# Optimization experiments

Hardware: AMD Instinct MI355X
Metric: run time of the kernel (lower is better)

The kernel has to match this reference:

```python
import jax, jax.numpy as jnp
import numpy as np

D_MODEL, D_STATE, D_CONV, EXPAND = 1024, 16, 4, 2
D_INNER = D_MODEL * EXPAND
BATCH, SEQ_LEN = 2, 2048
LN_EPS = 1e-5


def setup_inputs() -> dict:
    key = jax.random.key(0)
    ks = jax.random.split(key, 10)
    s = lambda fan_in: 1.0 / np.sqrt(fan_in)
    x = jax.random.normal(ks[0], (BATCH, D_MODEL, SEQ_LEN), jnp.float32)
    ln_w = jnp.ones((D_MODEL,), jnp.float32)
    ln_b = jnp.zeros((D_MODEL,), jnp.float32)
    # Linear weights stored as [in, out]
    W_in = jax.random.normal(ks[1], (D_MODEL, 2 * D_INNER), jnp.float32) * s(D_MODEL)
    conv_w = jax.random.normal(ks[2], (D_INNER, 1, D_CONV), jnp.float32) * s(D_CONV)
    conv_b = jax.random.normal(ks[3], (D_INNER,), jnp.float32) * s(D_CONV)
    W_x = jax.random.normal(ks[4], (D_INNER, 2 * D_STATE + D_INNER), jnp.float32) * s(D_INNER)
    W_dt = jax.random.normal(ks[5], (D_INNER, D_INNER), jnp.float32) * s(D_INNER)
    b_dt = jax.random.normal(ks[6], (D_INNER,), jnp.float32) * s(D_INNER)
    A_log = jnp.broadcast_to(jnp.log(jnp.arange(1, D_STATE + 1, dtype=jnp.float32))[None, :], (D_INNER, D_STATE))
    Dskip = jnp.ones((D_INNER,), jnp.float32)
    W_out = jax.random.normal(ks[7], (D_INNER, D_MODEL), jnp.float32) * s(D_INNER)
    return {"x": x, "ln_w": ln_w, "ln_b": ln_b, "W_in": W_in, "conv_w": conv_w,
            "conv_b": conv_b, "W_x": W_x, "W_dt": W_dt, "b_dt": b_dt,
            "A_log": A_log, "Dskip": Dskip, "W_out": W_out}


def _selective_scan(u, delta, A, Bp, Cp, Dskip):
    # u, delta: [B, d_inner, L]; A: [d_inner, d_state]; Bp, Cp: [B, d_state, L]
    u_T = jnp.transpose(u, (2, 0, 1))        # [L, B, d_inner]
    d_T = jnp.transpose(delta, (2, 0, 1))    # [L, B, d_inner]
    B_T = jnp.transpose(Bp, (2, 0, 1))       # [L, B, d_state]
    C_T = jnp.transpose(Cp, (2, 0, 1))       # [L, B, d_state]
    h0 = jnp.zeros((u.shape[0], u.shape[1], A.shape[1]), u.dtype)

    def step(h, inp):
        dlt_t, B_t, C_t, u_t = inp
        dA = jnp.exp(dlt_t[..., None] * A)                       # [B, d_inner, d_state]
        h = dA * h + dlt_t[..., None] * B_t[:, None, :] * u_t[..., None]
        y_t = jnp.einsum('bds,bs->bd', h, C_t)
        return h, y_t

    _, ys = jax.lax.scan(step, h0, (d_T, B_T, C_T, u_T))
    y = jnp.transpose(ys, (1, 2, 0))  # [B, d_inner, L]
    return y + Dskip[None, :, None] * u


def reference(x, ln_w, ln_b, W_in, conv_w, conv_b, W_x, W_dt, b_dt, A_log, Dskip, W_out):
    residual = x
    xt = jnp.swapaxes(x, 1, 2)  # [B, L, d_model]
    mu = xt.mean(-1, keepdims=True)
    var = ((xt - mu) ** 2).mean(-1, keepdims=True)
    xn = (xt - mu) * jax.lax.rsqrt(var + LN_EPS) * ln_w + ln_b
    xz = xn @ W_in                                   # [B, L, 2*d_inner]
    xb, z = jnp.split(xz, 2, axis=-1)
    xb = jnp.swapaxes(xb, 1, 2)                      # [B, d_inner, L]
    # causal depthwise conv (torch pads d_conv-1 both sides then slices [:L])
    xb = jax.lax.conv_general_dilated(
        xb, conv_w, window_strides=(1,), padding=[(D_CONV - 1, 0)],
        dimension_numbers=('NCH', 'OIH', 'NCH'), feature_group_count=D_INNER)
    xb = xb + conv_b[None, :, None]
    xb = jax.nn.silu(xb)
    xbt = jnp.swapaxes(xb, 1, 2)                     # [B, L, d_inner]
    bcd = xbt @ W_x                                  # [B, L, 2*d_state + d_inner]
    Bp = bcd[..., :D_STATE]
    Cp = bcd[..., D_STATE:2 * D_STATE]
    dlt = jax.nn.softplus(bcd[..., 2 * D_STATE:] @ W_dt + b_dt)
    Bp = jnp.swapaxes(Bp, 1, 2)                      # [B, d_state, L]
    Cp = jnp.swapaxes(Cp, 1, 2)
    dlt = jnp.swapaxes(dlt, 1, 2)                    # [B, d_inner, L]
    A = -jnp.exp(A_log)
    y = _selective_scan(xb, dlt, A, Bp, Cp, Dskip)   # [B, d_inner, L]
    y = jnp.swapaxes(y, 1, 2) * jax.nn.silu(z)       # [B, L, d_inner]
    out = y @ W_out                                  # [B, L, d_model]
    return jnp.swapaxes(out, 1, 2) + residual
```

## Files before the change

kernel.cpp:

```cpp
#include <hip/hip_runtime.h>
#include <cstdint>
#include <cstddef>

#define SEQL 2048
#define DMODEL 1024
#define DINNER 2048
#define NSTATE 16
#define NC 32
#define TC 64
#define KS 16
#define KCH 128

typedef __attribute__((ext_vector_type(4))) float f32x4;
typedef __attribute__((ext_vector_type(8))) short short8;
typedef __attribute__((ext_vector_type(4))) short short4v;
typedef unsigned short u16;

__device__ __forceinline__ float b2f(u16 u) {
  union { unsigned int i; float f; } v; v.i = ((unsigned int)u) << 16; return v.f;
}
__device__ __forceinline__ u16 f2b(float f) {
  union { float f; unsigned int i; } v; v.f = f;
  unsigned int r = v.i + 0x7FFFu + ((v.i >> 16) & 1u);
  return (u16)(r >> 16);
}

__global__ __launch_bounds__(256) void k_transpose_cvt(
    const float* __restrict__ in, u16* __restrict__ out, int R, int C, int c0) {
  __shared__ float t[32][33];
  int cb = blockIdx.x * 32, rb = blockIdx.y * 32;
  int tx = threadIdx.x, ty = threadIdx.y;
#pragma unroll
  for (int i = 0; i < 32; i += 8)
    t[ty + i][tx] = in[(size_t)(rb + ty + i) * C + c0 + cb + tx];
  __syncthreads();
#pragma unroll
  for (int i = 0; i < 32; i += 8)
    out[(size_t)(cb + ty + i) * R + rb + tx] = f2b(t[tx][ty + i]);
}

__global__ __launch_bounds__(256) void k_cvt_rows(
    const float* __restrict__ in, u16* __restrict__ out) {
  size_t idx = (size_t)blockIdx.x * 256 + threadIdx.x;
  size_t i4 = idx * 4;
  int r = (int)(i4 >> 11), c = (int)(i4 & 2047);
  f32x4 v = *(const f32x4*)&in[(size_t)r * 2080 + 32 + c];
  short4v o;
#pragma unroll
  for (int j = 0; j < 4; ++j) o[j] = (short)f2b(v[j]);
  *(short4v*)&out[i4] = o;
}

__global__ __launch_bounds__(256) void k_layernorm(
    const u16* __restrict__ xt, const float* __restrict__ w,
    const float* __restrict__ b, u16* __restrict__ xn) {
  int row = blockIdx.x;
  const u16* px = xt + (size_t)row * DMODEL;
  int i4 = threadIdx.x * 4;
  short4v sv = *(const short4v*)&px[i4];
  float v[4];
#pragma unroll
  for (int j = 0; j < 4; ++j) v[j] = b2f((u16)sv[j]);
  float s1 = v[0] + v[1] + v[2] + v[3];
  float s2 = v[0]*v[0] + v[1]*v[1] + v[2]*v[2] + v[3]*v[3];
#pragma unroll
  for (int off = 32; off > 0; off >>= 1) {
    s1 += __shfl_xor(s1, off);
    s2 += __shfl_xor(s2, off);
  }
  __shared__ float a1[4], a2[4];
  int lane = threadIdx.x & 63, wid = threadIdx.x >> 6;
  if (lane == 0) { a1[wid] = s1; a2[wid] = s2; }
  __syncthreads();
  float t1 = a1[0] + a1[1] + a1[2] + a1[3];
  float t2 = a2[0] + a2[1] + a2[2] + a2[3];
  float mu = t1 * (1.f / DMODEL);
  float rs = rsqrtf(t2 * (1.f / DMODEL) - mu * mu + 1e-5f);
  short4v ov;
#pragma unroll
  for (int j = 0; j < 4; ++j) ov[j] = (short)f2b((v[j] - mu) * rs * w[i4 + j] + b[i4 + j]);
  *(short4v*)&xn[(size_t)row * DMODEL + i4] = ov;
}

template<int EPI>
__global__ __launch_bounds__(256) void gemm8p(
    const u16* __restrict__ A, const u16* __restrict__ BT,
    void* __restrict__ outp, const float* __restrict__ bias,
    const float* __restrict__ resid, int M, int N, int K) {
  constexpr int LDSTILE = 2 * 128 * 64;
  __shared__ u16 lds[2 * LDSTILE];

  const int tid = threadIdx.x;
  const int w = tid >> 6, lane = tid & 63;
  const int wm = w >> 1, wn = w & 1;
  const int lg = lane >> 4, lr = lane & 15;
  const int wbase = tid & ~63;

  const int gx = N / 128;
  const int cpx = gridDim.x >> 3;
  const int wg = ((int)blockIdx.x & 7) * cpx + ((int)blockIdx.x >> 3);
  const int tm = (wg / gx) * 128;
  const int tn = (wg % gx) * 128;
  const int NT = K >> 6;

  const u16* aSp[2];
  const u16* bSp[2];
  int aD[2], bD[2];
#pragma unroll
  for (int j = 0; j < 2; ++j) {
    int t8 = j * 256 + tid;
    int r8 = t8 >> 3;
    int pr = (r8 & 31) + ((r8 >> 5) << 6);
    int sk = ((((t8 & 7) << 4) ^ ((pr & 7) << 4)) >> 1);
    aSp[j] = A + (size_t)(tm + pr) * K + sk;
    bSp[j] = BT + (size_t)(tn + pr) * K + sk;
    int r8b = (j * 256 + wbase) >> 3;
    int prb = (r8b & 31) + ((r8b >> 5) << 6);
    aD[j] = prb * 64;
    bD[j] = 128 * 64 + prb * 64;
  }
  int aFo[4][2], bFo[4][2];
#pragma unroll
  for (int mf = 0; mf < 4; ++mf)
#pragma unroll
    for (int kk = 0; kk < 2; ++kk) {
      int r = wm * 64 + mf * 16 + lr;
      aFo[mf][kk] = r * 128 + ((kk * 64 + lg * 16) ^ ((r & 7) << 4));
      int rb = wn * 64 + mf * 16 + lr;
      bFo[mf][kk] = 128 * 64 * 2 + rb * 128 + ((kk * 64 + lg * 16) ^ ((rb & 7) << 4));
    }

  auto stA = [&](int toff, int h, int buf) {
#pragma unroll
    for (int j = 0; j < 2; ++j)
      __builtin_amdgcn_global_load_lds(
          (const __attribute__((address_space(1))) void*)(aSp[j] + toff * 64 + h * (K << 5)),
          (__attribute__((address_space(3))) void*)(lds + buf * LDSTILE + aD[j] + h * 2048),
          16, 0, 0);
  };
  auto stB = [&](int toff, int h, int buf) {
#pragma unroll
    for (int j = 0; j < 2; ++j)
      __builtin_amdgcn_global_load_lds(
          (const __attribute__((address_space(1))) void*)(bSp[j] + toff * 64 + h * (K << 5)),
          (__attribute__((address_space(3))) void*)(lds + buf * LDSTILE + bD[j] + h * 2048),
          16, 0, 0);
  };

  f32x4 acc[4][4] = {};
  short8 aF[2][2], bF0[2][2], bF1[2][2];

  stA(0, 0, 0); stB(0, 0, 0); stB(0, 1, 0); stA(0, 1, 0);
  stA(1, 0, 1); stB(1, 0, 1);
  asm volatile("s_waitcnt vmcnt(4)" ::: "memory");
  __builtin_amdgcn_s_barrier();

  for (int tt = 0; tt < NT; tt += 2) {
#pragma unroll
    for (int u = 0; u < 2; ++u) {
      const char* Lb = (const char*)lds + u * (LDSTILE * 2);
#pragma unroll
      for (int mf = 0; mf < 2; ++mf)
#pragma unroll
        for (int kk = 0; kk < 2; ++kk) aF[mf][kk] = *(const short8*)(Lb + aFo[mf][kk]);
#pragma unroll
      for (int nf = 0; nf < 2; ++nf)
#pragma unroll
        for (int kk = 0; kk < 2; ++kk) bF0[nf][kk] = *(const short8*)(Lb + bFo[nf][kk]);
      stB(u + 1, 1, (u + 1) & 1);
      __builtin_amdgcn_s_barrier();
      asm volatile("s_waitcnt lgkmcnt(0)" ::: "memory");
      __builtin_amdgcn_s_setprio(1);
#pragma unroll
      for (int mf = 0; mf < 2; ++mf)
#pragma unroll
        for (int nf = 0; nf < 2; ++nf) {
          acc[mf][nf] = __builtin_amdgcn_mfma_f32_16x16x32_bf16(aF[mf][0], bF0[nf][0], acc[mf][nf], 0, 0, 0);
          acc[mf][nf] = __builtin_amdgcn_mfma_f32_16x16x32_bf16(aF[mf][1], bF0[nf][1], acc[mf][nf], 0, 0, 0);
        }
      __builtin_amdgcn_s_setprio(0);
      __builtin_amdgcn_s_barrier();
#pragma unroll
      for (int nf = 0; nf < 2; ++nf)
#pragma unroll
        for (int kk = 0; kk < 2; ++kk) bF1[nf][kk] = *(const short8*)(Lb + bFo[2 + nf][kk]);
      stA(u + 1, 1, (u + 1) & 1);
      __builtin_amdgcn_s_barrier();
      asm volatile("s_waitcnt lgkmcnt(0)" ::: "memory");
      __builtin_amdgcn_s_setprio(1);
#pragma unroll
      for (int mf = 0; mf < 2; ++mf)
#pragma unroll
        for (int nf = 0; nf < 2; ++nf) {
          acc[mf][2 + nf] = __builtin_amdgcn_mfma_f32_16x16x32_bf16(aF[mf][0], bF1[nf][0], acc[mf][2 + nf], 0, 0, 0);
          acc[mf][2 + nf] = __builtin_amdgcn_mfma_f32_16x16x32_bf16(aF[mf][1], bF1[nf][1], acc[mf][2 + nf], 0, 0, 0);
        }
      __builtin_amdgcn_s_setprio(0);
      __builtin_amdgcn_s_barrier();
#pragma unroll
      for (int mf = 0; mf < 2; ++mf)
#pragma unroll
        for (int kk = 0; kk < 2; ++kk) aF[mf][kk] = *(const short8*)(Lb + aFo[2 + mf][kk]);
      stA(u + 2, 0, u & 1);
      __builtin_amdgcn_s_barrier();
      asm volatile("s_waitcnt lgkmcnt(0)" ::: "memory");
      __builtin_amdgcn_s_setprio(1);
#pragma unroll
      for (int mf = 0; mf < 2; ++mf)
#pragma unroll
        for (int nf = 0; nf < 2; ++nf) {
          acc[2 + mf][nf] = __builtin_amdgcn_mfma_f32_16x16x32_bf16(aF[mf][0], bF0[nf][0], acc[2 + mf][nf], 0, 0, 0);
          acc[2 + mf][nf] = __builtin_amdgcn_mfma_f32_16x16x32_bf16(aF[mf][1], bF0[nf][1], acc[2 + mf][nf], 0, 0, 0);
        }
      __builtin_amdgcn_s_setprio(0);
      __builtin_amdgcn_s_barrier();
      stB(u + 2, 0, u & 1);
      __builtin_amdgcn_s_barrier();
      asm volatile("s_waitcnt lgkmcnt(0)" ::: "memory");
      __builtin_amdgcn_s_setprio(1);
#pragma unroll
      for (int mf = 0; mf < 2; ++mf)
#pragma unroll
        for (int nf = 0; nf < 2; ++nf) {
          acc[2 + mf][2 + nf] = __builtin_amdgcn_mfma_f32_16x16x32_bf16(aF[mf][0], bF1[nf][0], acc[2 + mf][2 + nf], 0, 0, 0);
          acc[2 + mf][2 + nf] = __builtin_amdgcn_mfma_f32_16x16x32_bf16(aF[mf][1], bF1[nf][1], acc[2 + mf][2 + nf], 0, 0, 0);
        }
      __builtin_amdgcn_s_setprio(0);
      asm volatile("s_waitcnt vmcnt(4)" ::: "memory");
      __builtin_amdgcn_s_barrier();
    }
#pragma unroll
    for (int j = 0; j < 2; ++j) { aSp[j] += 128; bSp[j] += 128; }
  }

#pragma unroll
  for (int mf = 0; mf < 4; ++mf) {
    int r0 = tm + wm * 64 + mf * 16 + lg * 4;
#pragma unroll
    for (int nf = 0; nf < 4; ++nf) {
      int c = tn + wn * 64 + nf * 16 + lr;
      f32x4 v = acc[mf][nf];
#pragma unroll
      for (int j = 0; j < 4; ++j) {
        int r = r0 + j;
        if constexpr (EPI == 1) {
          ((u16*)outp)[(size_t)r * N + c] = f2b(v[j]);
        } else if constexpr (EPI == 2) {
          float xv = v[j] + bias[c];
          ((float*)outp)[(size_t)r * N + c] = (xv > 20.f) ? xv : log1pf(__expf(xv));
        } else if constexpr (EPI == 3) {
          int bb = r >> 11, tt2 = r & (SEQL - 1);
          size_t oi = ((size_t)(bb * N + c)) * SEQL + tt2;
          ((float*)outp)[oi] = v[j] + resid[oi];
        } else {
          ((float*)outp)[(size_t)r * N + c] = v[j];
        }
      }
    }
  }
}

__global__ __launch_bounds__(256) void k_conv_silu(
    const u16* __restrict__ xz, const float* __restrict__ cw,
    const float* __restrict__ cb, u16* __restrict__ xbt) {
  size_t idx = (size_t)blockIdx.x * 256 + threadIdx.x;
  int d2 = (int)(idx & (DINNER / 2 - 1));
  int d = d2 * 2;
  int l = (int)((idx >> 10) & (SEQL - 1));
  int b = (int)(idx >> 21);
  f32x4 w0 = *(const f32x4*)&cw[d * 4];
  f32x4 w1 = *(const f32x4*)&cw[d * 4 + 4];
  float a0 = cb[d], a1 = cb[d + 1];
  size_t base = ((size_t)b * SEQL + l) * 4096 + d;
#pragma unroll
  for (int i = 0; i < 4; ++i) {
    int ls = l - 3 + i;
    if (ls >= 0) {
      unsigned int pv = *(const unsigned int*)&xz[base + (size_t)(i - 3) * 4096];
      a0 += w0[i] * b2f((u16)(pv & 0xFFFF));
      a1 += w1[i] * b2f((u16)(pv >> 16));
    }
  }
  float s0 = a0 / (1.f + __expf(-a0));
  float s1 = a1 / (1.f + __expf(-a1));
  unsigned int ov = (unsigned int)f2b(s0) | ((unsigned int)f2b(s1) << 16);
  *(unsigned int*)&xbt[((size_t)b * SEQL + l) * DINNER + d] = ov;
}

__global__ __launch_bounds__(256) void k_bc_mfma(
    const u16* __restrict__ xbt, const u16* __restrict__ WxBCT,
    float* __restrict__ bcp) {
  __shared__ u16 As[128 * 32];
  int tid = threadIdx.x;
  int w = tid >> 6, lane = tid & 63;
  int tm = blockIdx.x * 128;
  int k0 = blockIdx.y * KCH;
  int lg = lane >> 4, lr = lane & 15;
  int srow = lane >> 2, scol = (lane & 3) * 8;

  f32x4 acc[2][2] = {};

  for (int kk = k0; kk < k0 + KCH; kk += 32) {
#pragma unroll
    for (int j = 0; j < 2; ++j) {
      int ch = w * 2 + j;
      const u16* ga = xbt + (size_t)(tm + ch * 16 + srow) * DINNER + kk + scol;
      __builtin_amdgcn_global_load_lds(
          (const __attribute__((address_space(1))) void*)ga,
          (__attribute__((address_space(3))) void*)&As[ch * 512], 16, 0, 0);
    }
    __syncthreads();
    short8 aF[2], bF[2];
#pragma unroll
    for (int m = 0; m < 2; ++m)
      aF[m] = *(const short8*)&As[(w * 32 + m * 16 + lr) * 32 + lg * 8];
#pragma unroll
    for (int n = 0; n < 2; ++n)
      bF[n] = *(const short8*)&WxBCT[(size_t)(n * 16 + lr) * DINNER + kk + lg * 8];
#pragma unroll
    for (int m = 0; m < 2; ++m)
#pragma unroll
      for (int n = 0; n < 2; ++n)
        acc[m][n] = __builtin_amdgcn_mfma_f32_16x16x32_bf16(aF[m], bF[n], acc[m][n], 0, 0, 0);
    __syncthreads();
  }

  float* outp = bcp + (size_t)blockIdx.y * (4096 * 32);
#pragma unroll
  for (int m = 0; m < 2; ++m) {
    int r0 = tm + w * 32 + m * 16 + lg * 4;
#pragma unroll
    for (int n = 0; n < 2; ++n) {
      int c = n * 16 + lr;
      f32x4 v = acc[m][n];
#pragma unroll
      for (int j = 0; j < 4; ++j)
        outp[(size_t)(r0 + j) * 32 + c] = v[j];
    }
  }
}

__global__ __launch_bounds__(256) void k_bc_red(
    const float* __restrict__ bcp, float* __restrict__ bc) {
  size_t i = (size_t)blockIdx.x * 256 + threadIdx.x;
  float s = 0.f;
#pragma unroll
  for (int ks = 0; ks < KS; ++ks)
    s += bcp[(size_t)ks * (4096 * 32) + i];
  bc[i] = s;
}

__global__ __launch_bounds__(256) void k_scan_p1(
    const float* __restrict__ dlt, const u16* __restrict__ ub,
    const float* __restrict__ bcv, const float* __restrict__ A_log,
    float* __restrict__ Pc, float* __restrict__ Qc) {
  int d = blockIdx.x * 256 + threadIdx.x;
  int c = blockIdx.y;
  int b = blockIdx.z;
  float Av[16];
#pragma unroll
  for (int sv = 0; sv < 4; ++sv) {
    f32x4 al = *(const f32x4*)&A_log[d * 16 + sv * 4];
#pragma unroll
    for (int j = 0; j < 4; ++j) Av[sv * 4 + j] = -__expf(al[j]);
  }
  float P[16], Q[16];
#pragma unroll
  for (int s = 0; s < 16; ++s) { P[s] = 1.f; Q[s] = 0.f; }
  size_t row0 = (size_t)b * SEQL + (size_t)c * TC;
  for (int t = 0; t < TC; ++t) {
    size_t row = row0 + t;
    float dl = dlt[row * DINNER + d];
    float uu = b2f(ub[row * DINNER + d]);
    float bco = dl * uu;
    const f32x4* Bp = (const f32x4*)&bcv[row * 32];
#pragma unroll
    for (int sv = 0; sv < 4; ++sv) {
      f32x4 Bv = Bp[sv];
#pragma unroll
      for (int j = 0; j < 4; ++j) {
        int s = sv * 4 + j;
        float dA = __expf(dl * Av[s]);
        P[s] *= dA;
        Q[s] = dA * Q[s] + bco * Bv[j];
      }
    }
  }
  size_t base = (((size_t)b * NC + c) * DINNER + d) * 16;
#pragma unroll
  for (int sv = 0; sv < 4; ++sv) {
    f32x4 pv, qv;
#pragma unroll
    for (int j = 0; j < 4; ++j) { pv[j] = P[sv * 4 + j]; qv[j] = Q[sv * 4 + j]; }
    *(f32x4*)&Pc[base + sv * 4] = pv;
    *(f32x4*)&Qc[base + sv * 4] = qv;
  }
}

__global__ __launch_bounds__(256) void k_scan_p2(
    const float* __restrict__ Pc, const float* __restrict__ Qc,
    float* __restrict__ Hs) {
  size_t gid = (size_t)blockIdx.x * 256 + threadIdx.x;
  size_t bds = gid & ((size_t)DINNER * 16 - 1);
  int b = (int)(gid >> 15);
  float h = 0.f;
  size_t cstride = (size_t)DINNER * 16;
  size_t base = (size_t)b * NC * cstride + bds;
  for (int c = 0; c < NC; ++c) {
    size_t idx = base + (size_t)c * cstride;
    Hs[idx] = h;
    h = Pc[idx] * h + Qc[idx];
  }
}

__global__ __launch_bounds__(256) void k_scan_p3(
    const float* __restrict__ dlt, const u16* __restrict__ ub,
    const float* __restrict__ bcv, const u16* __restrict__ xz,
    const float* __restrict__ A_log, const float* __restrict__ Dskip,
    const float* __restrict__ Hs, u16* __restrict__ yg) {
  int d = blockIdx.x * 256 + threadIdx.x;
  int c = blockIdx.y;
  int b = blockIdx.z;
  float Av[16];
#pragma unroll
  for (int sv = 0; sv < 4; ++sv) {
    f32x4 al = *(const f32x4*)&A_log[d * 16 + sv * 4];
#pragma unroll
    for (int j = 0; j < 4; ++j) Av[sv * 4 + j] = -__expf(al[j]);
  }
  float h[16];
  size_t hb = (((size_t)b * NC + c) * DINNER + d) * 16;
#pragma unroll
  for (int sv = 0; sv < 4; ++sv) {
    f32x4 hv = *(const f32x4*)&Hs[hb + sv * 4];
#pragma unroll
    for (int j = 0; j < 4; ++j) h[sv * 4 + j] = hv[j];
  }
  float Dsk = Dskip[d];
  size_t row0 = (size_t)b * SEQL + (size_t)c * TC;
  for (int t = 0; t < TC; ++t) {
    size_t row = row0 + t;
    float dl = dlt[row * DINNER + d];
    float uu = b2f(ub[row * DINNER + d]);
    float bco = dl * uu;
    const f32x4* BCp = (const f32x4*)&bcv[row * 32];
    float y = 0.f;
#pragma unroll
    for (int sv = 0; sv < 4; ++sv) {
      f32x4 Bv = BCp[sv];
      f32x4 Cv = BCp[4 + sv];
#pragma unroll
      for (int j = 0; j < 4; ++j) {
        int s = sv * 4 + j;
        float dA = __expf(dl * Av[s]);
        h[s] = dA * h[s] + bco * Bv[j];
        y += h[s] * Cv[j];
      }
    }
    float zv = b2f(xz[row * 4096 + DINNER + d]);
    float yv = (y + Dsk * uu) * (zv / (1.f + __expf(-zv)));
    yg[row * DINNER + d] = f2b(yv);
  }
}

extern "C" void kernel_launch(void* const* d_in, const int* in_sizes, int n_in,
                              void* d_out, int out_size, void* d_ws, size_t ws_size,
                              hipStream_t stream) {
  (void)in_sizes; (void)n_in; (void)out_size; (void)ws_size;
  const float* x      = (const float*)d_in[0];
  const float* ln_w   = (const float*)d_in[1];
  const float* ln_b   = (const float*)d_in[2];
  const float* W_in   = (const float*)d_in[3];
  const float* conv_w = (const float*)d_in[4];
  const float* conv_b = (const float*)d_in[5];
  const float* W_x    = (const float*)d_in[6];
  const float* W_dt   = (const float*)d_in[7];
  const float* b_dt   = (const float*)d_in[8];
  const float* A_log  = (const float*)d_in[9];
  const float* Dskip  = (const float*)d_in[10];
  const float* W_out  = (const float*)d_in[11];
  float* out = (float*)d_out;

  char* ws = (char*)d_ws;
  const size_t MB = 1048576;
  u16*  xt    = (u16*)(ws + 0 * MB);
  u16*  xn    = (u16*)(ws + 8 * MB);
  u16*  WinT  = (u16*)(ws + 16 * MB);
  u16*  WdtT  = (u16*)(ws + 32 * MB);
  u16*  WoutT = (u16*)(ws + 40 * MB);
  u16*  xz    = (u16*)(ws + 44 * MB);
  u16*  xbt   = (u16*)(ws + 76 * MB);
  float* bc   = (float*)(ws + 92 * MB);
  u16*  WxRaw = (u16*)(ws + 93 * MB);
  u16*  W_cT  = (u16*)(ws + 101 * MB);
  float* dlt  = (float*)(ws + 109 * MB);
  float* Pc   = (float*)(ws + 141 * MB);
  float* Qc   = (float*)(ws + 149 * MB);
  float* Hs   = (float*)(ws + 157 * MB);
  float* bcp  = (float*)(ws + 165 * MB);
  u16*  WxBCT = (u16*)(ws + 173 * MB);
  u16*  yg    = (u16*)(ws + 0 * MB);

  dim3 tb(32, 8);
  for (int b = 0; b < 2; ++b)
    k_transpose_cvt<<<dim3(SEQL / 32, DMODEL / 32), tb, 0, stream>>>(
        x + (size_t)b * DMODEL * SEQL, xt + (size_t)b * SEQL * DMODEL, DMODEL, SEQL, 0);
  k_transpose_cvt<<<dim3(4096 / 32, 1024 / 32), tb, 0, stream>>>(W_in, WinT, 1024, 4096, 0);
  k_transpose_cvt<<<dim3(1, 2048 / 32), tb, 0, stream>>>(W_x, WxBCT, 2048, 2080, 0);
  k_transpose_cvt<<<dim3(2048 / 32, 2048 / 32), tb, 0, stream>>>(W_dt, WdtT, 2048, 2048, 0);
  k_transpose_cvt<<<dim3(1024 / 32, 2048 / 32), tb, 0, stream>>>(W_out, WoutT, 2048, 1024, 0);
  k_cvt_rows<<<4096, 256, 0, stream>>>(W_x, WxRaw);

  gemm8p<1><<<256, 256, 0, stream>>>(WdtT, WxRaw, W_cT, nullptr, nullptr, 2048, 2048, 2048);

  k_layernorm<<<4096, 256, 0, stream>>>(xt, ln_w, ln_b, xn);

  gemm8p<1><<<1024, 256, 0, stream>>>(xn, WinT, xz, nullptr, nullptr, 4096, 4096, 1024);

  k_conv_silu<<<16384, 256, 0, stream>>>(xz, conv_w, conv_b, xbt);

  k_bc_mfma<<<dim3(4096 / 128, KS), 256, 0, stream>>>(xbt, WxBCT, bcp);
  k_bc_red<<<131072 / 256, 256, 0, stream>>>(bcp, bc);

  gemm8p<2><<<512, 256, 0, stream>>>(xbt, W_cT, dlt, b_dt, nullptr, 4096, 2048, 2048);

  k_scan_p1<<<dim3(DINNER / 256, NC, 2), 256, 0, stream>>>(dlt, xbt, bc, A_log, Pc, Qc);
  k_scan_p2<<<256, 256, 0, stream>>>(Pc, Qc, Hs);
  k_scan_p3<<<dim3(DINNER / 256, NC, 2), 256, 0, stream>>>(
      dlt, xbt, bc, xz, A_log, Dskip, Hs, yg);

  gemm8p<3><<<256, 256, 0, stream>>>(yg, WoutT, out, nullptr, x, 4096, 1024, 2048);
}
```

Before: 310.9 us.

## Use 256x256-tile 512-thread GEMM for in-projection and store delta as bf16

Adds a new GEMM kernel with 256x256 output tiles, 8 waves and double-buffered direct-to-LDS loads, and uses it for the xn @ W_in projection in place of the 128x128-tile kernel. The larger tile raises arithmetic intensity and cuts global reloads of A and B. The grid is only 256 blocks, which roughly matches the CU count, so there is little latency hiding per CU. Separately, the softplus delta output is now stored as bf16 instead of fp32, halving that tensor's traffic into the two scan passes at some cost in precision.

```diff
diff --git a/kernel.cpp b/kernel.cpp
--- a/kernel.cpp
+++ b/kernel.cpp
@@ -80,6 +80,160 @@
 #pragma unroll
   for (int j = 0; j < 4; ++j) ov[j] = (short)f2b((v[j] - mu) * rs * w[i4 + j] + b[i4 + j]);
   *(short4v*)&xn[(size_t)row * DMODEL + i4] = ov;
+}
+
+__global__ __launch_bounds__(512) void gemm8x(
+    const u16* __restrict__ A, const u16* __restrict__ BT,
+    u16* __restrict__ outp, int M, int N, int K) {
+  constexpr int LDSTILE = 64 * 512;
+  __shared__ u16 lds[2 * LDSTILE];
+
+  const int tid = threadIdx.x;
+  const int w = tid >> 6, lane = tid & 63;
+  const int wm = w >> 2, wn = w & 3;
+  const int lg = lane >> 4, lr = lane & 15;
+  const int wbase = tid & ~63;
+
+  const int gx = N / 256;
+  const int cpx = gridDim.x >> 3;
+  const int wg = ((int)blockIdx.x & 7) * cpx + ((int)blockIdx.x >> 3);
+  const int tm = (wg / gx) * 256;
+  const int tn = (wg % gx) * 256;
+  const int NT = K >> 6;
+
+  const u16* Ab = A + (size_t)tm * K;
+  const u16* Bb = BT + (size_t)tn * K;
+
+  auto stageA = [&](int tc, int h) {
+    int tcl = tc < NT ? tc : NT - 1;
+    const u16* g0 = Ab + (size_t)tcl * 64;
+    u16* l0 = lds + (tc & 1) * LDSTILE;
+#pragma unroll
+    for (int j = 0; j < 2; ++j) {
+      int t8 = j * 512 + tid;
+      int r8 = t8 >> 3;
+      int pr = (r8 & 63) + ((r8 >> 6) << 7) + h * 64;
+      int sk = ((((t8 & 7) << 4) ^ ((pr & 7) << 4)) >> 1);
+      int r8b = (j * 512 + wbase) >> 3;
+      int prb = (r8b & 63) + ((r8b >> 6) << 7) + h * 64;
+      __builtin_amdgcn_global_load_lds(
+          (const __attribute__((address_space(1))) void*)(g0 + (size_t)pr * K + sk),
+          (__attribute__((address_space(3))) void*)(l0 + prb * 64), 16, 0, 0);
+    }
+  };
+  auto stageB = [&](int tc, int h) {
+    int tcl = tc < NT ? tc : NT - 1;
+    const u16* g0 = Bb + (size_t)tcl * 64;
+    u16* l0 = lds + (tc & 1) * LDSTILE + 256 * 64;
+#pragma unroll
+    for (int j = 0; j < 2; ++j) {
+      int t8 = j * 512 + tid;
+      int r8 = t8 >> 3;
+      int pr = (r8 % 32) + (r8 / 32) * 64 + h * 32;
+      int sk = ((((t8 & 7) << 4) ^ ((pr & 7) << 4)) >> 1);
+      int r8b = (j * 512 + wbase) >> 3;
+      int prb = (r8b % 32) + (r8b / 32) * 64 + h * 32;
+      __builtin_amdgcn_global_load_lds(
+          (const __attribute__((address_space(1))) void*)(g0 + (size_t)pr * K + sk),
+          (__attribute__((address_space(3))) void*)(l0 + prb * 64), 16, 0, 0);
+    }
+  };
+  auto fragA = [&](const u16* base, int mf, int kk) -> short8 {
+    int r = wm * 128 + mf * 16 + lr;
+    int cb = (kk * 64 + lg * 16) ^ ((r & 7) << 4);
+    return *(const short8*)((const char*)base + r * 128 + cb);
+  };
+  auto fragB = [&](const u16* base, int nf, int kk) -> short8 {
+    int r = wn * 64 + nf * 16 + lr;
+    int cb = (kk * 64 + lg * 16) ^ ((r & 7) << 4);
+    return *(const short8*)((const char*)base + 256 * 128 + r * 128 + cb);
+  };
+
+  f32x4 acc[8][4] = {};
+  short8 aF[4][2], bF0[2][2], bF1[2][2];
+
+  stageA(0, 0); stageB(0, 0); stageB(0, 1); stageA(0, 1);
+  stageA(1, 0); stageB(1, 0);
+  asm volatile("s_waitcnt vmcnt(4)" ::: "memory");
+  __builtin_amdgcn_s_barrier();
+
+  for (int t = 0; t < NT; ++t) {
+    const u16* Ac = lds + (t & 1) * LDSTILE;
+#pragma unroll
+    for (int mf = 0; mf < 4; ++mf) { aF[mf][0] = fragA(Ac, mf, 0); aF[mf][1] = fragA(Ac, mf, 1); }
+#pragma unroll
+    for (int nf = 0; nf < 2; ++nf) { bF0[nf][0] = fragB(Ac, nf, 0); bF0[nf][1] = fragB(Ac, nf, 1); }
+    stageB(t + 1, 1);
+    __builtin_amdgcn_s_barrier();
+    asm volatile("s_waitcnt lgkmcnt(0)" ::: "memory");
+    __builtin_amdgcn_s_setprio(1);
+#pragma unroll
+    for (int mf = 0; mf < 4; ++mf)
+#pragma unroll
+      for (int nf = 0; nf < 2; ++nf) {
+        acc[mf][nf] = __builtin_amdgcn_mfma_f32_16x16x32_bf16(aF[mf][0], bF0[nf][0], acc[mf][nf], 0, 0, 0);
+        acc[mf][nf] = __builtin_amdgcn_mfma_f32_16x16x32_bf16(aF[mf][1], bF0[nf][1], acc[mf][nf], 0, 0, 0);
+      }
+    __builtin_amdgcn_s_setprio(0);
+    __builtin_amdgcn_s_barrier();
+#pragma unroll
+    for (int nf = 0; nf < 2; ++nf) { bF1[nf][0] = fragB(Ac, 2 + nf, 0); bF1[nf][1] = fragB(Ac, 2 + nf, 1); }
+    stageA(t + 1, 1);
+    __builtin_amdgcn_s_barrier();
+    asm volatile("s_waitcnt lgkmcnt(0)" ::: "memory");
+    __builtin_amdgcn_s_setprio(1);
+#pragma unroll
+    for (int mf = 0; mf < 4; ++mf)
+#pragma unroll
+      for (int nf = 0; nf < 2; ++nf) {
+        acc[mf][2 + nf] = __builtin_amdgcn_mfma_f32_16x16x32_bf16(aF[mf][0], bF1[nf][0], acc[mf][2 + nf], 0, 0, 0);
+        acc[mf][2 + nf] = __builtin_amdgcn_mfma_f32_16x16x32_bf16(aF[mf][1], bF1[nf][1], acc[mf][2 + nf], 0, 0, 0);
+      }
+    __builtin_amdgcn_s_setprio(0);
+    __builtin_amdgcn_s_barrier();
+#pragma unroll
+    for (int mf = 0; mf < 4; ++mf) { aF[mf][0] = fragA(Ac, 4 + mf, 0); aF[mf][1] = fragA(Ac, 4 + mf, 1); }
+    stageA(t + 2, 0);
+    __builtin_amdgcn_s_barrier();
+    asm volatile("s_waitcnt lgkmcnt(0)" ::: "memory");
+    __builtin_amdgcn_s_setprio(1);
+#pragma unroll
+    for (int mf = 0; mf < 4; ++mf)
+#pragma unroll
+      for (int nf = 0; nf < 2; ++nf) {
+        acc[4 + mf][nf] = __builtin_amdgcn_mfma_f32_16x16x32_bf16(aF[mf][0], bF0[nf][0], acc[4 + mf][nf], 0, 0, 0);
+        acc[4 + mf][nf] = __builtin_amdgcn_mfma_f32_16x16x32_bf16(aF[mf][1], bF0[nf][1], acc[4 + mf][nf], 0, 0, 0);
+      }
+    __builtin_amdgcn_s_setprio(0);
+    __builtin_amdgcn_s_barrier();
+    stageB(t + 2, 0);
+    __builtin_amdgcn_s_barrier();
+    asm volatile("s_waitcnt lgkmcnt(0)" ::: "memory");
+    __builtin_amdgcn_s_setprio(1);
+#pragma unroll
+    for (int mf = 0; mf < 4; ++mf)
+#pragma unroll
+      for (int nf = 0; nf < 2; ++nf) {
+        acc[4 + mf][2 + nf] = __builtin_amdgcn_mfma_f32_16x16x32_bf16(aF[mf][0], bF1[nf][0], acc[4 + mf][2 + nf], 0, 0, 0);
+        acc[4 + mf][2 + nf] = __builtin_amdgcn_mfma_f32_16x16x32_bf16(aF[mf][1], bF1[nf][1], acc[4 + mf][2 + nf], 0, 0, 0);
+      }
+    __builtin_amdgcn_s_setprio(0);
+    asm volatile("s_waitcnt vmcnt(4)" ::: "memory");
+    __builtin_amdgcn_s_barrier();
+  }
+
+#pragma unroll
+  for (int mf = 0; mf < 8; ++mf) {
+    int r0 = tm + wm * 128 + mf * 16 + lg * 4;
+#pragma unroll
+    for (int nf = 0; nf < 4; ++nf) {
+      int c = tn + wn * 64 + nf * 16 + lr;
+      f32x4 v = acc[mf][nf];
+#pragma unroll
+      for (int j = 0; j < 4; ++j)
+        outp[(size_t)(r0 + j) * N + c] = f2b(v[j]);
+    }
+  }
 }
 
 template<int EPI>
@@ -238,22 +392,23 @@
     int r0 = tm + wm * 64 + mf * 16 + lg * 4;
 #pragma unroll
     for (int nf = 0; nf < 4; ++nf) {
-      int c = tn + wn * 64 + nf * 16 + lr;
+      int c2 = tn + wn * 64 + nf * 16 + lr;
       f32x4 v = acc[mf][nf];
 #pragma unroll
       for (int j = 0; j < 4; ++j) {
         int r = r0 + j;
         if constexpr (EPI == 1) {
-          ((u16*)outp)[(size_t)r * N + c] = f2b(v[j]);
+          ((u16*)outp)[(size_t)r * N + c2] = f2b(v[j]);
         } else if constexpr (EPI == 2) {
-          float xv = v[j] + bias[c];
-          ((float*)outp)[(size_t)r * N + c] = (xv > 20.f) ? xv : log1pf(__expf(xv));
+          float xv = v[j] + bias[c2];
+          float sp = (xv > 20.f) ? xv : log1pf(__expf(xv));
+          ((u16*)outp)[(size_t)r * N + c2] = f2b(sp);
         } else if constexpr (EPI == 3) {
           int bb = r >> 11, tt2 = r & (SEQL - 1);
-          size_t oi = ((size_t)(bb * N + c)) * SEQL + tt2;
+          size_t oi = ((size_t)(bb * N + c2)) * SEQL + tt2;
           ((float*)outp)[oi] = v[j] + resid[oi];
         } else {
-          ((float*)outp)[(size_t)r * N + c] = v[j];
+          ((float*)outp)[(size_t)r * N + c2] = v[j];
         }
       }
     }
@@ -351,7 +506,7 @@
 }
 
 __global__ __launch_bounds__(256) void k_scan_p1(
-    const float* __restrict__ dlt, const u16* __restrict__ ub,
+    const u16* __restrict__ dlt, const u16* __restrict__ ub,
     const float* __restrict__ bcv, const float* __restrict__ A_log,
     float* __restrict__ Pc, float* __restrict__ Qc) {
   int d = blockIdx.x * 256 + threadIdx.x;
@@ -370,7 +525,7 @@
   size_t row0 = (size_t)b * SEQL + (size_t)c * TC;
   for (int t = 0; t < TC; ++t) {
     size_t row = row0 + t;
-    float dl = dlt[row * DINNER + d];
+    float dl = b2f(dlt[row * DINNER + d]);
     float uu = b2f(ub[row * DINNER + d]);
     float bco = dl * uu;
     const f32x4* Bp = (const f32x4*)&bcv[row * 32];
@@ -414,7 +569,7 @@
 }
 
 __global__ __launch_bounds__(256) void k_scan_p3(
-    const float* __restrict__ dlt, const u16* __restrict__ ub,
+    const u16* __restrict__ dlt, const u16* __restrict__ ub,
     const float* __restrict__ bcv, const u16* __restrict__ xz,
     const float* __restrict__ A_log, const float* __restrict__ Dskip,
     const float* __restrict__ Hs, u16* __restrict__ yg) {
@@ -440,7 +595,7 @@
   size_t row0 = (size_t)b * SEQL + (size_t)c * TC;
   for (int t = 0; t < TC; ++t) {
     size_t row = row0 + t;
-    float dl = dlt[row * DINNER + d];
+    float dl = b2f(dlt[row * DINNER + d]);
     float uu = b2f(ub[row * DINNER + d]);
     float bco = dl * uu;
     const f32x4* BCp = (const f32x4*)&bcv[row * 32];
@@ -493,7 +648,7 @@
   float* bc   = (float*)(ws + 92 * MB);
   u16*  WxRaw = (u16*)(ws + 93 * MB);
   u16*  W_cT  = (u16*)(ws + 101 * MB);
-  float* dlt  = (float*)(ws + 109 * MB);
+  u16*  dlt   = (u16*)(ws + 109 * MB);
   float* Pc   = (float*)(ws + 141 * MB);
   float* Qc   = (float*)(ws + 149 * MB);
   float* Hs   = (float*)(ws + 157 * MB);
@@ -515,7 +670,7 @@
 
   k_layernorm<<<4096, 256, 0, stream>>>(xt, ln_w, ln_b, xn);
 
-  gemm8p<1><<<1024, 256, 0, stream>>>(xn, WinT, xz, nullptr, nullptr, 4096, 4096, 1024);
+  gemm8x<<<256, 512, 0, stream>>>(xn, WinT, xz, 4096, 4096, 1024);
 
   k_conv_silu<<<16384, 256, 0, stream>>>(xz, conv_w, conv_b, xbt);
 
```

Result: no change. 306.3 us (median of 2 runs) (-1.5%).
